# Performance work log

Measured on AMD Instinct MI355X. Metric: run time of the kernel, lower is better.

## Reference

```python
import jax, jax.numpy as jnp
import numpy as np

NUM_NODES = 4904
EMBED_DIM = 300
NUM_CLASSES = 14


def setup_inputs() -> dict:
    key = jax.random.key(0)
    k1, k2, k3, k4, k5, k6, k7, k8 = jax.random.split(key, 8)
    B, L, K = 128, 512, 8
    master_nodes = jax.random.randint(k1, (B, L), 0, NUM_NODES + 1)
    slave_nodes = jax.random.randint(k2, (B, L, K), 0, NUM_NODES + 1)
    slave_edges = jax.random.randint(k3, (B, L, K), 0, NUM_NODES * NUM_NODES + 1)
    # Embedding tables (padding_idx=0 -> zero row)
    R = jax.random.normal(k4, (NUM_NODES + 1, EMBED_DIM), dtype=jnp.float32)
    R = R.at[0].set(0.0)
    E = jax.random.normal(k5, (NUM_NODES * NUM_NODES + 1, 1), dtype=jnp.float32)
    E = E.at[0].set(0.0)
    N = jax.random.normal(k6, (NUM_NODES + 1, 1), dtype=jnp.float32)
    N = N.at[0].set(0.0)
    # fc: Linear(300 -> 14)
    bound = 1.0 / np.sqrt(EMBED_DIM)
    W = jax.random.uniform(k7, (NUM_CLASSES, EMBED_DIM), minval=-bound, maxval=bound, dtype=jnp.float32)
    b = jax.random.uniform(k8, (NUM_CLASSES,), minval=-bound, maxval=bound, dtype=jnp.float32)
    return {"master_nodes": master_nodes, "slave_nodes": slave_nodes,
            "slave_edges": slave_edges, "R": R, "E": E, "N": N, "W": W, "b": b}


def reference(master_nodes, slave_nodes, slave_edges, R, E, N, W, b):
    Rn = R[master_nodes]          # [B, L, D]
    Ra = R[slave_nodes]           # [B, L, K, D]
    Ean = E[slave_edges]          # [B, L, K, 1]
    Mn = jnp.max(Ra * Ean, axis=2)  # [B, L, D] max-pool over neighbors
    Nn = N[master_nodes]          # [B, L, 1] gate
    x = (1.0 - Nn) * Mn + Nn * Rn  # [B, L, D]
    x = jnp.sum(x, axis=1)         # [B, D]
    h = jax.nn.relu(x @ W.T + b)   # [B, C]
    # Dropout is identity in eval mode; softmax over classes (dim=1)
    return jax.nn.softmax(h, axis=1)
```

## Files before the change

kernel.cpp:

```cpp
#include <hip/hip_runtime.h>
#include <math.h>

#define BB 128
#define LL 512
#define KK 8
#define DD 300
#define D2 150
#define CC 14
#define L_PER_BLOCK 16

__global__ __launch_bounds__(256) void gather_en(
    const int* __restrict__ edges, const float* __restrict__ E,
    const int* __restrict__ master, const float* __restrict__ N,
    float* __restrict__ e_ws, float* __restrict__ nn_ws)
{
    const int i = blockIdx.x * 256 + threadIdx.x;
    e_ws[i] = E[edges[i]];
    if (i < BB * LL) nn_ws[i] = N[master[i]];
}

__global__ __launch_bounds__(192) void gnn_agg(
    const int* __restrict__ master, const int* __restrict__ slaves,
    const float2* __restrict__ R2, const float* __restrict__ e_ws,
    const float* __restrict__ nn_ws, float* __restrict__ X)
{
    const int b  = blockIdx.x;
    const int lc = blockIdx.y;
    const int t  = threadIdx.x;
    const bool act = (t < D2);

    float accx = 0.f, accy = 0.f;
    const int bl_base = b * LL + lc * L_PER_BLOCK;

    for (int li = 0; li < L_PER_BLOCK; li += 2) {
        const int bl0 = bl_base + li;
        const int bl1 = bl0 + 1;

        const int   m0 = master[bl0], m1 = master[bl1];
        const float n0 = nn_ws[bl0],  n1 = nn_ws[bl1];
        int   s0[KK], s1[KK];
        float e0[KK], e1[KK];
#pragma unroll
        for (int k = 0; k < KK; ++k) { s0[k] = slaves[bl0*KK+k]; s1[k] = slaves[bl1*KK+k]; }
#pragma unroll
        for (int k = 0; k < KK; ++k) { e0[k] = e_ws[bl0*KK+k];  e1[k] = e_ws[bl1*KK+k]; }

        if (act) {
            float2 r0[KK], r1[KK];
#pragma unroll
            for (int k = 0; k < KK; ++k) r0[k] = R2[s0[k]*D2 + t];
#pragma unroll
            for (int k = 0; k < KK; ++k) r1[k] = R2[s1[k]*D2 + t];
            const float2 rm0 = R2[m0*D2 + t];
            const float2 rm1 = R2[m1*D2 + t];

            float mx0 = r0[0].x * e0[0], my0 = r0[0].y * e0[0];
            float mx1 = r1[0].x * e1[0], my1 = r1[0].y * e1[0];
#pragma unroll
            for (int k = 1; k < KK; ++k) {
                mx0 = fmaxf(mx0, r0[k].x * e0[k]);
                my0 = fmaxf(my0, r0[k].y * e0[k]);
                mx1 = fmaxf(mx1, r1[k].x * e1[k]);
                my1 = fmaxf(my1, r1[k].y * e1[k]);
            }
            accx += (1.f - n0) * mx0 + n0 * rm0.x;
            accy += (1.f - n0) * my0 + n0 * rm0.y;
            accx += (1.f - n1) * mx1 + n1 * rm1.x;
            accy += (1.f - n1) * my1 + n1 * rm1.y;
        }
    }
    if (act) {
        atomicAdd(&X[b * DD + 2*t],     accx);
        atomicAdd(&X[b * DD + 2*t + 1], accy);
    }
}

__global__ __launch_bounds__(256) void fc_softmax(
    const float* __restrict__ X, const float* __restrict__ W,
    const float* __restrict__ bias, float* __restrict__ out)
{
    const int b = blockIdx.x;
    const int t = threadIdx.x;
    const int c = t >> 4;
    const int j = t & 15;
    __shared__ float h[CC];

    if (c < CC) {
        float acc = 0.f;
        const float* x = X + b * DD;
        const float* w = W + c * DD;
        for (int d = j; d < DD; d += 16) acc += x[d] * w[d];
#pragma unroll
        for (int off = 8; off > 0; off >>= 1) acc += __shfl_down(acc, off, 16);
        if (j == 0) h[c] = fmaxf(acc + bias[c], 0.f);
    }
    __syncthreads();
    if (t < CC) {
        float mx = -INFINITY;
#pragma unroll
        for (int i = 0; i < CC; ++i) mx = fmaxf(mx, h[i]);
        float s = 0.f;
#pragma unroll
        for (int i = 0; i < CC; ++i) s += expf(h[i] - mx);
        out[b * CC + t] = expf(h[t] - mx) / s;
    }
}

extern "C" void kernel_launch(void* const* d_in, const int* in_sizes, int n_in,
                              void* d_out, int out_size, void* d_ws, size_t ws_size,
                              hipStream_t stream) {
    const int*   master = (const int*)d_in[0];
    const int*   slaves = (const int*)d_in[1];
    const int*   edges  = (const int*)d_in[2];
    const float* R      = (const float*)d_in[3];
    const float* E      = (const float*)d_in[4];
    const float* N      = (const float*)d_in[5];
    const float* W      = (const float*)d_in[6];
    const float* bias   = (const float*)d_in[7];
    float* out = (float*)d_out;

    float* X     = (float*)d_ws;
    float* nn_ws = X + BB * DD;
    float* e_ws  = nn_ws + BB * LL;

    hipMemsetAsync(X, 0, BB * DD * sizeof(float), stream);

    gather_en<<<(BB * LL * KK) / 256, 256, 0, stream>>>(edges, E, master, N, e_ws, nn_ws);

    dim3 grid(BB, LL / L_PER_BLOCK);
    gnn_agg<<<grid, 192, 0, stream>>>(master, slaves, (const float2*)R, e_ws, nn_ws, X);

    fc_softmax<<<BB, 256, 0, stream>>>(X, W, bias, out);
}
```

Before: 223.7 us.

## Convert R to fp16 copy, pack per-node index records, fuse prep kernels

```diff
diff --git a/kernel.cpp b/kernel.cpp
--- a/kernel.cpp
+++ b/kernel.cpp
@@ -1,4 +1,5 @@
 #include <hip/hip_runtime.h>
+#include <hip/hip_fp16.h>
 #include <math.h>
 
 #define BB 128
@@ -8,21 +9,39 @@
 #define D2 150
 #define CC 14
 #define L_PER_BLOCK 16
+#define UNROLL 4
 
-__global__ __launch_bounds__(256) void gather_en(
-    const int* __restrict__ edges, const float* __restrict__ E,
-    const int* __restrict__ master, const float* __restrict__ N,
-    float* __restrict__ e_ws, float* __restrict__ nn_ws)
+#define R_H2_ELEMS ((4905 * 300) / 2)
+#define REC_INTS 20
+
+__global__ __launch_bounds__(256) void prep(
+    const float2* __restrict__ R, const int* __restrict__ edges,
+    const float* __restrict__ E, const int* __restrict__ master,
+    const float* __restrict__ N, const int* __restrict__ slaves,
+    __half2* __restrict__ R16, int* __restrict__ rec, float* __restrict__ X)
 {
     const int i = blockIdx.x * 256 + threadIdx.x;
-    e_ws[i] = E[edges[i]];
-    if (i < BB * LL) nn_ws[i] = N[master[i]];
+
+    if (i < R_H2_ELEMS) {
+        const float2 f = R[i];
+        R16[i] = __floats2half2_rn(f.x, f.y);
+    }
+    if (i < BB * LL * KK) {
+        const int bl = i >> 3, k = i & 7;
+        rec[bl * REC_INTS + 2 + 2 * k] = slaves[i] * D2;
+        rec[bl * REC_INTS + 3 + 2 * k] = __float_as_int(E[edges[i]]);
+    }
+    if (i < BB * LL) {
+        const int m = master[i];
+        rec[i * REC_INTS]     = m * D2;
+        rec[i * REC_INTS + 1] = __float_as_int(N[m]);
+    }
+    if (i < BB * DD) X[i] = 0.f;
 }
 
 __global__ __launch_bounds__(192) void gnn_agg(
-    const int* __restrict__ master, const int* __restrict__ slaves,
-    const float2* __restrict__ R2, const float* __restrict__ e_ws,
-    const float* __restrict__ nn_ws, float* __restrict__ X)
+    const int4* __restrict__ rec4, const __half2* __restrict__ R16,
+    float* __restrict__ X)
 {
     const int b  = blockIdx.x;
     const int lc = blockIdx.y;
@@ -32,41 +51,54 @@
     float accx = 0.f, accy = 0.f;
     const int bl_base = b * LL + lc * L_PER_BLOCK;
 
-    for (int li = 0; li < L_PER_BLOCK; li += 2) {
-        const int bl0 = bl_base + li;
-        const int bl1 = bl0 + 1;
+    for (int lg = 0; lg < L_PER_BLOCK; lg += UNROLL) {
+        int   offm[UNROLL], offs[UNROLL][KK];
+        float nn[UNROLL], e[UNROLL][KK];
 
-        const int   m0 = master[bl0], m1 = master[bl1];
-        const float n0 = nn_ws[bl0],  n1 = nn_ws[bl1];
-        int   s0[KK], s1[KK];
-        float e0[KK], e1[KK];
 #pragma unroll
-        for (int k = 0; k < KK; ++k) { s0[k] = slaves[bl0*KK+k]; s1[k] = slaves[bl1*KK+k]; }
-#pragma unroll
-        for (int k = 0; k < KK; ++k) { e0[k] = e_ws[bl0*KK+k];  e1[k] = e_ws[bl1*KK+k]; }
+        for (int u = 0; u < UNROLL; ++u) {
+            const int4* r = rec4 + (long)(bl_base + lg + u) * (REC_INTS / 4);
+            const int4 q0 = r[0];
+            const int4 q1 = r[1];
+            const int4 q2 = r[2];
+            const int4 q3 = r[3];
+            const int4 q4 = r[4];
+            offm[u] = q0.x;            nn[u]   = __int_as_float(q0.y);
+            offs[u][0] = q0.z;         e[u][0] = __int_as_float(q0.w);
+            offs[u][1] = q1.x;         e[u][1] = __int_as_float(q1.y);
+            offs[u][2] = q1.z;         e[u][2] = __int_as_float(q1.w);
+            offs[u][3] = q2.x;         e[u][3] = __int_as_float(q2.y);
+            offs[u][4] = q2.z;         e[u][4] = __int_as_float(q2.w);
+            offs[u][5] = q3.x;         e[u][5] = __int_as_float(q3.y);
+            offs[u][6] = q3.z;         e[u][6] = __int_as_float(q3.w);
+            offs[u][7] = q4.x;         e[u][7] = __int_as_float(q4.y);
+        }
 
         if (act) {
-            float2 r0[KK], r1[KK];
+            __half2 r[UNROLL][KK], rm[UNROLL];
 #pragma unroll
-            for (int k = 0; k < KK; ++k) r0[k] = R2[s0[k]*D2 + t];
+            for (int u = 0; u < UNROLL; ++u) {
 #pragma unroll
-            for (int k = 0; k < KK; ++k) r1[k] = R2[s1[k]*D2 + t];
-            const float2 rm0 = R2[m0*D2 + t];
-            const float2 rm1 = R2[m1*D2 + t];
+                for (int k = 0; k < KK; ++k) r[u][k] = R16[offs[u][k] + t];
+            }
+#pragma unroll
+            for (int u = 0; u < UNROLL; ++u) rm[u] = R16[offm[u] + t];
 
-            float mx0 = r0[0].x * e0[0], my0 = r0[0].y * e0[0];
-            float mx1 = r1[0].x * e1[0], my1 = r1[0].y * e1[0];
 #pragma unroll
-            for (int k = 1; k < KK; ++k) {
-                mx0 = fmaxf(mx0, r0[k].x * e0[k]);
-                my0 = fmaxf(my0, r0[k].y * e0[k]);
-                mx1 = fmaxf(mx1, r1[k].x * e1[k]);
-                my1 = fmaxf(my1, r1[k].y * e1[k]);
+            for (int u = 0; u < UNROLL; ++u) {
+                float2 f = __half22float2(r[u][0]);
+                float mx = f.x * e[u][0], my = f.y * e[u][0];
+#pragma unroll
+                for (int k = 1; k < KK; ++k) {
+                    f = __half22float2(r[u][k]);
+                    mx = fmaxf(mx, f.x * e[u][k]);
+                    my = fmaxf(my, f.y * e[u][k]);
+                }
+                const float2 rf = __half22float2(rm[u]);
+                const float n = nn[u], a = 1.f - nn[u];
+                accx = fmaf(a, mx, fmaf(n, rf.x, accx));
+                accy = fmaf(a, my, fmaf(n, rf.y, accy));
             }
-            accx += (1.f - n0) * mx0 + n0 * rm0.x;
-            accy += (1.f - n0) * my0 + n0 * rm0.y;
-            accx += (1.f - n1) * mx1 + n1 * rm1.x;
-            accy += (1.f - n1) * my1 + n1 * rm1.y;
         }
     }
     if (act) {
@@ -119,16 +151,16 @@
     const float* bias   = (const float*)d_in[7];
     float* out = (float*)d_out;
 
-    float* X     = (float*)d_ws;
-    float* nn_ws = X + BB * DD;
-    float* e_ws  = nn_ws + BB * LL;
+    char* ws = (char*)d_ws;
+    __half2* R16 = (__half2*)ws;
+    float*   X   = (float*)(ws + 2943104);
+    int*     rec = (int*)(ws + 2943104 + 153600);
 
-    hipMemsetAsync(X, 0, BB * DD * sizeof(float), stream);
-
-    gather_en<<<(BB * LL * KK) / 256, 256, 0, stream>>>(edges, E, master, N, e_ws, nn_ws);
+    prep<<<(R_H2_ELEMS + 255) / 256, 256, 0, stream>>>(
+        (const float2*)R, edges, E, master, N, slaves, R16, rec, X);
 
     dim3 grid(BB, LL / L_PER_BLOCK);
-    gnn_agg<<<grid, 192, 0, stream>>>(master, slaves, (const float2*)R, e_ws, nn_ws, X);
+    gnn_agg<<<grid, 192, 0, stream>>>((const int4*)rec, R16, X);
 
     fc_softmax<<<BB, 256, 0, stream>>>(X, W, bias, out);
 }
```

Measured after the change: 194.4 us. 13.1% less time.
